# Performance work log

Hardware: AMD Instinct MI355X
Metric: run time of the kernel (lower is better)

Reference implementation:

```python
import jax, jax.numpy as jnp
import numpy as np

B, C_IN, C_OUT, H, W = 4, 256, 256, 64, 64
K, STRIDE, PAD, DIL = 3, 1, 1, 1
KK = K * K


def setup_inputs() -> dict:
    key = jax.random.key(0)
    k1, k2, k3, k4 = jax.random.split(key, 4)
    x = jax.random.normal(k1, (B, C_IN, H, W), jnp.float32)
    # offset/mask conv weight (no bias), scaled small so offsets are modest
    w_mod = jax.random.normal(k2, (3 * KK, C_IN, K, K), jnp.float32) * 0.01
    # deform conv weight (xavier-ish scale) + bias
    w_def = jax.random.normal(k3, (C_OUT, C_IN, K, K), jnp.float32) * (1.0 / np.sqrt(C_IN * KK))
    b_def = jax.random.normal(k4, (C_OUT,), jnp.float32) * 0.01
    return {"x": x, "w_mod": w_mod, "w_def": w_def, "b_def": b_def}


def _conv_nchw(x, w, stride, pad):
    return jax.lax.conv_general_dilated(
        x, w, (stride, stride), [(pad, pad), (pad, pad)],
        dimension_numbers=("NCHW", "OIHW", "NCHW"))


def _bilinear_sample(x, py, px):
    # x: [B,C,H,W]; py/px: [B,KK,Ho,Wo] absolute sample coords (zero-pad outside)
    Bn, Cc, Hh, Ww = x.shape
    y0 = jnp.floor(py)
    x0 = jnp.floor(px)
    fy = py - y0
    fx = px - x0
    y0i = y0.astype(jnp.int32)
    x0i = x0.astype(jnp.int32)
    xf = x.reshape(Bn, Cc, Hh * Ww)

    def corner(yi, xi, wgt):
        valid = (yi >= 0) & (yi < Hh) & (xi >= 0) & (xi < Ww)
        yc = jnp.clip(yi, 0, Hh - 1)
        xc = jnp.clip(xi, 0, Ww - 1)
        idx = yc * Ww + xc                      # [B,KK,Ho,Wo]
        g = jax.vmap(lambda f, i: f[:, i])(xf, idx)  # [B,C,KK,Ho,Wo]
        return g * (wgt * valid)[:, None]

    return (corner(y0i, x0i, (1 - fy) * (1 - fx))
            + corner(y0i, x0i + 1, (1 - fy) * fx)
            + corner(y0i + 1, x0i, fy * (1 - fx))
            + corner(y0i + 1, x0i + 1, fy * fx))


def reference(x, w_mod, w_def, b_def):
    # offset/mask head
    mod = _conv_nchw(x, w_mod, STRIDE, PAD)          # [B, 3*KK, Ho, Wo]
    o1, o2, mask = mod[:, :KK], mod[:, KK:2 * KK], mod[:, 2 * KK:]
    offset = jnp.concatenate([o1, o2], axis=1)        # [B, 2*KK, Ho, Wo]
    # torchvision DeformConv2d: offset channels are interleaved (y, x) pairs
    dy = offset[:, 0::2]
    dx = offset[:, 1::2]
    mask = jax.nn.sigmoid(mask)                       # [B, KK, Ho, Wo]

    Ho, Wo = mod.shape[2], mod.shape[3]
    ky, kx = jnp.meshgrid(jnp.arange(K), jnp.arange(K), indexing="ij")
    ky = ky.reshape(-1).astype(jnp.float32)
    kx = kx.reshape(-1).astype(jnp.float32)
    base_y = (jnp.arange(Ho, dtype=jnp.float32) * STRIDE - PAD)[None, :, None] + (ky * DIL)[:, None, None]  # [KK,Ho,1]
    base_x = (jnp.arange(Wo, dtype=jnp.float32) * STRIDE - PAD)[None, None, :] + (kx * DIL)[:, None, None]  # [KK,1,Wo]
    py = dy + base_y[None]                            # [B,KK,Ho,Wo]
    px = dx + base_x[None]

    sampled = _bilinear_sample(x, py, px) * mask[:, None]  # [B,C,KK,Ho,Wo]
    out = jnp.einsum("bckhw,ock->bohw", sampled, w_def.reshape(C_OUT, C_IN, KK))
    return out + b_def[None, :, None, None]
```

## Files before the change

kernel.cpp:

```cpp
#include <hip/hip_runtime.h>

typedef unsigned short u16;
typedef unsigned int u32;
typedef short bf16x8 __attribute__((ext_vector_type(8)));
typedef float f32x4 __attribute__((ext_vector_type(4)));

#define CIN 256
#define COUT 256

__device__ __forceinline__ u16 f2b(float f) {
  u32 u = __float_as_uint(f);
  u += 0x7fffu + ((u >> 16) & 1u);
  return (u16)(u >> 16);
}
__device__ __forceinline__ u32 packbf(float lo, float hi) {
  return (u32)f2b(lo) | ((u32)f2b(hi) << 16);
}
__device__ __forceinline__ u32 bil2(u32 u00, u32 u01, u32 u10, u32 u11, float4 wt) {
  float s0 = __uint_as_float(u00 << 16) * wt.x;
  s0 = fmaf(__uint_as_float(u01 << 16), wt.y, s0);
  s0 = fmaf(__uint_as_float(u10 << 16), wt.z, s0);
  s0 = fmaf(__uint_as_float(u11 << 16), wt.w, s0);
  float s1 = __uint_as_float(u00 & 0xffff0000u) * wt.x;
  s1 = fmaf(__uint_as_float(u01 & 0xffff0000u), wt.y, s1);
  s1 = fmaf(__uint_as_float(u10 & 0xffff0000u), wt.z, s1);
  s1 = fmaf(__uint_as_float(u11 & 0xffff0000u), wt.w, s1);
  return packbf(s0, s1);
}
__device__ __forceinline__ void bar() {
  asm volatile("s_waitcnt lgkmcnt(0)\n\ts_barrier" ::: "memory");
}

__global__ __launch_bounds__(256) void k_prep(
    const float* __restrict__ x, const float* __restrict__ w_mod,
    const float* __restrict__ w_def,
    u16* __restrict__ xT, u16* __restrict__ Wm2, u16* __restrict__ W2) {
  __shared__ __align__(16) char SB[9216];
  int t = threadIdx.x, g = blockIdx.x;
  if (g < 1024) {
    u16 (*T)[72] = (u16(*)[72])SB;
    int b = g >> 8, ct = (g >> 6) & 3, pt = g & 63;
    int c0 = ct << 6, pos0 = pt << 6;
    {
      int cl = t >> 2, pb = (t & 3) << 4;
      const float* p = x + (((b << 8) + c0 + cl) << 12) + pos0 + pb;
#pragma unroll
      for (int i = 0; i < 4; ++i) {
        float4 v = *(const float4*)(p + i * 4);
        int pp = pb + i * 4;
        T[pp][cl] = f2b(v.x); T[pp + 1][cl] = f2b(v.y);
        T[pp + 2][cl] = f2b(v.z); T[pp + 3][cl] = f2b(v.w);
      }
    }
    __syncthreads();
    {
      int pl = t >> 2, q = t & 3;
      u16* dst = xT + (((b << 12) + pos0 + pl) << 8) + c0 + (q << 4);
      *(uint4*)dst = *(const uint4*)&T[pl][q << 4];
      *(uint4*)(dst + 8) = *(const uint4*)&T[pl][(q << 4) + 8];
    }
  } else {
    float* L = (float*)SB;
    int gg = g - 1024;
    if (gg < 256) {
      const float* src = w_def + gg * 2304;
      for (int j = t; j < 2304; j += 256) L[j] = src[j];
      __syncthreads();
      u16* dst = W2 + gg * 2304;
      for (int j = t; j < 2304; j += 256) {
        int kk = j >> 8, c = j & 255;
        dst[j] = f2b(L[c * 9 + kk]);
      }
    } else {
      int cm = gg - 256;
      if (cm < 27) {
        const float* src = w_mod + cm * 2304;
        for (int j = t; j < 2304; j += 256) L[j] = src[j];
      }
      __syncthreads();
      u16* dst = Wm2 + cm * 2304;
      for (int j = t; j < 2304; j += 256) {
        int kk = j >> 8, c = j & 255;
        dst[j] = (cm < 27) ? f2b(L[c * 9 + kk]) : (u16)0;
      }
    }
  }
}

__global__ __launch_bounds__(512) void k_modconv(
    const u16* __restrict__ xT, const u16* __restrict__ Wm2,
    int2* __restrict__ cidx, float4* __restrict__ cwt) {
  __shared__ __align__(16) u16 As[2][2][64][72];
  __shared__ float mods2[2][32][66];
  int t = threadIdx.x;
  int l = t & 63;
  int w = t >> 6;
  int h = t >> 8;
  int wl = w & 3;
  int tg = t & 255;
  int px = tg >> 2, q = tg & 3;
  int g = blockIdx.x;
  int b = (g & 7) >> 1, y = ((g >> 3) << 1) + (g & 1);
  const u16* xTb = xT + (b << 20);
  f32x4 zero = {0.f, 0.f, 0.f, 0.f};
  f32x4 acc0 = zero, acc1 = zero;
  int ml = l & 15, kq = l >> 4;

  uint4 VA0, VA1, VB0, VB1;
  uint4 S0, S1, S2, S3, T0, T1, T2, T3;

#define MC_ISSUE_A(i, V0, V1)                                                \
  { int ch_ = h * 18 + (i); int kk_ = ch_ >> 2, c0_ = (ch_ & 3) << 6;        \
    int ky_ = kk_ / 3, kx_ = kk_ - 3 * ky_;                                  \
    int ys_ = y + ky_ - 1, xs_ = px + kx_ - 1;                               \
    V0 = make_uint4(0, 0, 0, 0); V1 = V0;                                    \
    if (ys_ >= 0 && ys_ < 64 && xs_ >= 0 && xs_ < 64) {                      \
      const u16* p_ = xTb + (((ys_ << 6) + xs_) << 8) + c0_ + (q << 4);      \
      V0 = *(const uint4*)p_; V1 = *(const uint4*)(p_ + 8);                  \
    } }

#define MC_ISSUE_B(i, R0, R1, R2, R3)                                        \
  { int ch_ = h * 18 + (i); int kk_ = ch_ >> 2, c0_ = (ch_ & 3) << 6;        \
    const u16* pw_ = Wm2 + (kk_ << 8) + c0_ + (kq << 3);                     \
    R0 = *(const uint4*)(pw_ + ml * 2304);                                   \
    R1 = *(const uint4*)(pw_ + (16 + ml) * 2304);                            \
    R2 = *(const uint4*)(pw_ + ml * 2304 + 32);                              \
    R3 = *(const uint4*)(pw_ + (16 + ml) * 2304 + 32); }

#define MC_WRITE(buf, V0, V1)                                                \
  { *(uint4*)&As[h][buf][px][q << 4] = V0;                                   \
    *(uint4*)&As[h][buf][px][(q << 4) + 8] = V1; }

#define MC_MFMA(buf, R0, R1, R2, R3)                                         \
  { bf16x8 a0_ = *(const bf16x8*)&As[h][buf][wl * 16 + ml][kq << 3];         \
    acc0 = __builtin_amdgcn_mfma_f32_16x16x32_bf16(a0_, *(const bf16x8*)&R0, acc0, 0,0,0); \
    acc1 = __builtin_amdgcn_mfma_f32_16x16x32_bf16(a0_, *(const bf16x8*)&R1, acc1, 0,0,0); \
    bf16x8 a1_ = *(const bf16x8*)&As[h][buf][wl * 16 + ml][32 + (kq << 3)];  \
    acc0 = __builtin_amdgcn_mfma_f32_16x16x32_bf16(a1_, *(const bf16x8*)&R2, acc0, 0,0,0); \
    acc1 = __builtin_amdgcn_mfma_f32_16x16x32_bf16(a1_, *(const bf16x8*)&R3, acc1, 0,0,0); }

  MC_ISSUE_A(0, VA0, VA1)
  MC_ISSUE_A(1, VB0, VB1)
  MC_ISSUE_B(0, S0, S1, S2, S3)
#pragma unroll 1
  for (int i2 = 0; i2 < 18; i2 += 2) {
    MC_WRITE(0, VA0, VA1)
    bar();
    if (i2 + 2 < 18) MC_ISSUE_A(i2 + 2, VA0, VA1)
    MC_ISSUE_B(i2 + 1, T0, T1, T2, T3)
    MC_MFMA(0, S0, S1, S2, S3)
    MC_WRITE(1, VB0, VB1)
    bar();
    if (i2 + 3 < 18) MC_ISSUE_A(i2 + 3, VB0, VB1)
    if (i2 + 2 < 18) MC_ISSUE_B(i2 + 2, S0, S1, S2, S3)
    MC_MFMA(1, T0, T1, T2, T3)
  }
#pragma unroll
  for (int r = 0; r < 4; ++r) {
    mods2[h][ml][wl * 16 + kq * 4 + r]      = acc0[r];
    mods2[h][16 + ml][wl * 16 + kq * 4 + r] = acc1[r];
  }
  __syncthreads();
  for (int i2 = t; i2 < 576; i2 += 512) {
    int kk = i2 >> 6, pxx_i = i2 & 63;
    float dy = mods2[0][2 * kk][pxx_i] + mods2[1][2 * kk][pxx_i];
    float dx = mods2[0][2 * kk + 1][pxx_i] + mods2[1][2 * kk + 1][pxx_i];
    float mv = mods2[0][18 + kk][pxx_i] + mods2[1][18 + kk][pxx_i];
    float msk = 1.f / (1.f + __expf(-mv));
    int ky = kk / 3, kx = kk - 3 * ky;
    float py  = dy + (float)(y + ky - 1);
    float pxx = dx + (float)(pxx_i + kx - 1);
    float y0f = floorf(py), x0f = floorf(pxx);
    float fy = py - y0f, fx = pxx - x0f;
    int y0 = (int)y0f, x0 = (int)x0f;
    float vy0 = (y0 >= 0 && y0 < 64) ? msk : 0.f;
    float vy1 = (y0 + 1 >= 0 && y0 + 1 < 64) ? msk : 0.f;
    float w00 = (1.f - fy) * (1.f - fx) * vy0;
    float w01 = (1.f - fy) * fx * vy0;
    float w10 = fy * (1.f - fx) * vy1;
    float w11 = fy * fx * vy1;
    int xb2 = min(max(x0, 0), 62);
    float wA0 = (xb2 == x0) ? w00 : ((xb2 == x0 + 1) ? w01 : 0.f);
    float wB0 = (xb2 + 1 == x0) ? w00 : ((xb2 + 1 == x0 + 1) ? w01 : 0.f);
    float wA1 = (xb2 == x0) ? w10 : ((xb2 == x0 + 1) ? w11 : 0.f);
    float wB1 = (xb2 + 1 == x0) ? w10 : ((xb2 + 1 == x0 + 1) ? w11 : 0.f);
    int ib0 = min(max(y0, 0), 63) * 64 + xb2;
    int ib1 = min(max(y0 + 1, 0), 63) * 64 + xb2;
    int ci = ((b * 9 + kk) << 12) + (y << 6) + pxx_i;
    cidx[ci] = make_int2(ib0, ib1);
    cwt[ci]  = make_float4(wA0, wB0, wA1, wB1);
  }
#undef MC_ISSUE_A
#undef MC_ISSUE_B
#undef MC_WRITE
#undef MC_MFMA
}

__global__ __launch_bounds__(512) void k_main(
    const u16* __restrict__ xT, const u16* __restrict__ W2,
    const float* __restrict__ b_def,
    const int2* __restrict__ cidx, const float4* __restrict__ cwt,
    float* __restrict__ out) {
  __shared__ __align__(16) u16 As[2][64][72];
  __shared__ __align__(16) int2 Cs_i[576];
  __shared__ __align__(16) float4 Cs_w[576];
  int t = threadIdx.x;
  int l = t & 63;
  int w = t >> 6;
  int g = blockIdx.x;
  int b = (g & 7) >> 1, y = ((g >> 3) << 1) + (g & 1);
  const u16* xTb = xT + (b << 20);
  int gm = t >> 3, go = t & 7;
  int ml = l & 15, kq = l >> 4;
  int nrow0 = w * 32 + ml, nrow1 = nrow0 + 16;

  f32x4 zero = {0.f, 0.f, 0.f, 0.f};
  f32x4 acc[4][2];
#pragma unroll
  for (int i = 0; i < 4; ++i) { acc[i][0] = zero; acc[i][1] = zero; }

  for (int i = t; i < 576; i += 512) {
    int kk = i >> 6, px = i & 63;
    int ci = ((b * 9 + kk) << 12) + (y << 6) + px;
    Cs_i[i] = cidx[ci];
    Cs_w[i] = cwt[ci];
  }
  bar();

  uint4 A00, A01, A02, A03; float4 wt0;
  uint4 A10, A11, A12, A13; float4 wt1;
  uint4 RA0, RA1, RA2, RA3;
  uint4 RB0, RB1, RB2, RB3;

#define ISSUE_A(chunk, a0, a1, a2, a3, wt)                                   \
  { int kk_ = (chunk) >> 2, c0_ = ((chunk) & 3) << 6;                        \
    int cI_ = (kk_ << 6) + gm;                                               \
    int2 ib_ = Cs_i[cI_];                                                    \
    wt = Cs_w[cI_];                                                          \
    const u16* p0_ = xTb + (ib_.x << 8) + c0_ + (go << 3);                   \
    const u16* p1_ = xTb + (ib_.y << 8) + c0_ + (go << 3);                   \
    a0 = *(const uint4*)p0_;  a1 = *(const uint4*)(p0_ + 256);               \
    a2 = *(const uint4*)p1_;  a3 = *(const uint4*)(p1_ + 256); }

#define ISSUE_B(chunk, R0, R1, R2, R3)                                       \
  { int kk_ = (chunk) >> 2, c0_ = ((chunk) & 3) << 6;                        \
    const u16* pw_ = W2 + (kk_ << 8) + c0_ + (kq << 3);                      \
    R0 = *(const uint4*)(pw_ + nrow0 * 2304);                                \
    R1 = *(const uint4*)(pw_ + nrow1 * 2304);                                \
    R2 = *(const uint4*)(pw_ + nrow0 * 2304 + 32);                           \
    R3 = *(const uint4*)(pw_ + nrow1 * 2304 + 32); }

#define UNPACK(CUR, a0, a1, a2, a3, wt)                                      \
  { u32 q0_ = bil2(a0.x, a1.x, a2.x, a3.x, wt);                              \
    u32 q1_ = bil2(a0.y, a1.y, a2.y, a3.y, wt);                              \
    u32 q2_ = bil2(a0.z, a1.z, a2.z, a3.z, wt);                              \
    u32 q3_ = bil2(a0.w, a1.w, a2.w, a3.w, wt);                              \
    *(uint4*)&As[CUR][gm][go << 3] = make_uint4(q0_, q1_, q2_, q3_); }

#define DOMFMA(CUR, R0, R1, R2, R3)                                          \
  { bf16x8 a0_ = *(const bf16x8*)&As[CUR][ml][kq << 3];                      \
    bf16x8 a1_ = *(const bf16x8*)&As[CUR][16 + ml][kq << 3];                 \
    bf16x8 a2_ = *(const bf16x8*)&As[CUR][32 + ml][kq << 3];                 \
    bf16x8 a3_ = *(const bf16x8*)&As[CUR][48 + ml][kq << 3];                 \
    bf16x8 b0_ = *(const bf16x8*)&R0;                                        \
    bf16x8 b1_ = *(const bf16x8*)&R1;                                        \
    acc[0][0] = __builtin_amdgcn_mfma_f32_16x16x32_bf16(a0_, b0_, acc[0][0], 0,0,0); \
    acc[1][0] = __builtin_amdgcn_mfma_f32_16x16x32_bf16(a1_, b0_, acc[1][0], 0,0,0); \
    acc[2][0] = __builtin_amdgcn_mfma_f32_16x16x32_bf16(a2_, b0_, acc[2][0], 0,0,0); \
    acc[3][0] = __builtin_amdgcn_mfma_f32_16x16x32_bf16(a3_, b0_, acc[3][0], 0,0,0); \
    acc[0][1] = __builtin_amdgcn_mfma_f32_16x16x32_bf16(a0_, b1_, acc[0][1], 0,0,0); \
    acc[1][1] = __builtin_amdgcn_mfma_f32_16x16x32_bf16(a1_, b1_, acc[1][1], 0,0,0); \
    acc[2][1] = __builtin_amdgcn_mfma_f32_16x16x32_bf16(a2_, b1_, acc[2][1], 0,0,0); \
    acc[3][1] = __builtin_amdgcn_mfma_f32_16x16x32_bf16(a3_, b1_, acc[3][1], 0,0,0); \
    a0_ = *(const bf16x8*)&As[CUR][ml][32 + (kq << 3)];                      \
    a1_ = *(const bf16x8*)&As[CUR][16 + ml][32 + (kq << 3)];                 \
    a2_ = *(const bf16x8*)&As[CUR][32 + ml][32 + (kq << 3)];                 \
    a3_ = *(const bf16x8*)&As[CUR][48 + ml][32 + (kq << 3)];                 \
    b0_ = *(const bf16x8*)&R2;                                               \
    b1_ = *(const bf16x8*)&R3;                                               \
    acc[0][0] = __builtin_amdgcn_mfma_f32_16x16x32_bf16(a0_, b0_, acc[0][0], 0,0,0); \
    acc[1][0] = __builtin_amdgcn_mfma_f32_16x16x32_bf16(a1_, b0_, acc[1][0], 0,0,0); \
    acc[2][0] = __builtin_amdgcn_mfma_f32_16x16x32_bf16(a2_, b0_, acc[2][0], 0,0,0); \
    acc[3][0] = __builtin_amdgcn_mfma_f32_16x16x32_bf16(a3_, b0_, acc[3][0], 0,0,0); \
    acc[0][1] = __builtin_amdgcn_mfma_f32_16x16x32_bf16(a0_, b1_, acc[0][1], 0,0,0); \
    acc[1][1] = __builtin_amdgcn_mfma_f32_16x16x32_bf16(a1_, b1_, acc[1][1], 0,0,0); \
    acc[2][1] = __builtin_amdgcn_mfma_f32_16x16x32_bf16(a2_, b1_, acc[2][1], 0,0,0); \
    acc[3][1] = __builtin_amdgcn_mfma_f32_16x16x32_bf16(a3_, b1_, acc[3][1], 0,0,0); }

  ISSUE_A(0, A00, A01, A02, A03, wt0)
  ISSUE_A(1, A10, A11, A12, A13, wt1)
  ISSUE_B(0, RA0, RA1, RA2, RA3)
#pragma unroll 1
  for (int c2 = 0; c2 < 36; c2 += 2) {
    UNPACK(0, A00, A01, A02, A03, wt0)
    bar();
    if (c2 + 2 < 36) ISSUE_A(c2 + 2, A00, A01, A02, A03, wt0)
    ISSUE_B(c2 + 1, RB0, RB1, RB2, RB3)
    DOMFMA(0, RA0, RA1, RA2, RA3)
    UNPACK(1, A10, A11, A12, A13, wt1)
    bar();
    if (c2 + 3 < 36) ISSUE_A(c2 + 3, A10, A11, A12, A13, wt1)
    if (c2 + 2 < 36) ISSUE_B(c2 + 2, RA0, RA1, RA2, RA3)
    DOMFMA(1, RB0, RB1, RB2, RB3)
  }

#pragma unroll
  for (int nt = 0; nt < 2; ++nt) {
    int n = w * 32 + nt * 16 + ml;
    float bias = b_def[n];
    float* op = out + (((b << 8) + n) << 12) + (y << 6);
#pragma unroll
    for (int mt = 0; mt < 4; ++mt) {
      float4 v;
      v.x = acc[mt][nt][0] + bias;
      v.y = acc[mt][nt][1] + bias;
      v.z = acc[mt][nt][2] + bias;
      v.w = acc[mt][nt][3] + bias;
      *(float4*)(op + mt * 16 + kq * 4) = v;
    }
  }
#undef ISSUE_A
#undef ISSUE_B
#undef UNPACK
#undef DOMFMA
}

extern "C" void kernel_launch(void* const* d_in, const int* in_sizes, int n_in,
                              void* d_out, int out_size, void* d_ws, size_t ws_size,
                              hipStream_t stream) {
  const float* x     = (const float*)d_in[0];
  const float* w_mod = (const float*)d_in[1];
  const float* w_def = (const float*)d_in[2];
  const float* b_def = (const float*)d_in[3];
  float* out = (float*)d_out;
  char* ws = (char*)d_ws;
  u16*    xT   = (u16*)(ws);
  u16*    W2   = (u16*)(ws + 8388608);
  u16*    Wm2  = (u16*)(ws + 8388608 + 1179648);
  int2*   cidx = (int2*)(ws + 8388608 + 1179648 + 147456);
  float4* cwt  = (float4*)(ws + 8388608 + 1179648 + 147456 + 1179648);

  hipLaunchKernelGGL(k_prep, dim3(1312), dim3(256), 0, stream, x, w_mod, w_def, xT, Wm2, W2);
  hipLaunchKernelGGL(k_modconv, dim3(256), dim3(512), 0, stream, xT, Wm2, cidx, cwt);
  hipLaunchKernelGGL(k_main, dim3(256), dim3(512), 0, stream, xT, W2, b_def, cidx, cwt, out);
}
```

Measured before the change: 158.2 us.

## Split output channels across two blocks to double k_main grid

k_main now launches 512 blocks instead of 256, and each block computes 128 output channels (16 per wave) instead of all 256. This gives more blocks per CU on a 256-CU part and halves the accumulator registers per wave. The cost is that the bilinear gather and unpack of the A tile is done twice, once per channel half, so global gather traffic and VALU work for sampling double. The workspace offsets are also moved into named constants, which does not change behaviour.

```diff
diff --git a/kernel.cpp b/kernel.cpp
--- a/kernel.cpp
+++ b/kernel.cpp
@@ -30,6 +30,12 @@
 __device__ __forceinline__ void bar() {
   asm volatile("s_waitcnt lgkmcnt(0)\n\ts_barrier" ::: "memory");
 }
+
+#define WS_XT    0u
+#define WS_W2    8388608u
+#define WS_WM2   9568256u
+#define WS_CIDX  9715712u
+#define WS_CWT   10895360u
 
 __global__ __launch_bounds__(256) void k_prep(
     const float* __restrict__ x, const float* __restrict__ w_mod,
@@ -208,16 +214,13 @@
   int l = t & 63;
   int w = t >> 6;
   int g = blockIdx.x;
-  int b = (g & 7) >> 1, y = ((g >> 3) << 1) + (g & 1);
+  int ns = g >> 8;
+  int r = g & 255;
+  int b = (r & 7) >> 1, y = ((r >> 3) << 1) + (r & 1);
   const u16* xTb = xT + (b << 20);
   int gm = t >> 3, go = t & 7;
   int ml = l & 15, kq = l >> 4;
-  int nrow0 = w * 32 + ml, nrow1 = nrow0 + 16;
-
-  f32x4 zero = {0.f, 0.f, 0.f, 0.f};
-  f32x4 acc[4][2];
-#pragma unroll
-  for (int i = 0; i < 4; ++i) { acc[i][0] = zero; acc[i][1] = zero; }
+  int nrow = ns * 128 + w * 16 + ml;
 
   for (int i = t; i < 576; i += 512) {
     int kk = i >> 6, px = i & 63;
@@ -225,12 +228,17 @@
     Cs_i[i] = cidx[ci];
     Cs_w[i] = cwt[ci];
   }
-  bar();
+  __syncthreads();
+
+  f32x4 zero = {0.f, 0.f, 0.f, 0.f};
+  f32x4 acc[4];
+#pragma unroll
+  for (int i = 0; i < 4; ++i) acc[i] = zero;
 
   uint4 A00, A01, A02, A03; float4 wt0;
   uint4 A10, A11, A12, A13; float4 wt1;
-  uint4 RA0, RA1, RA2, RA3;
-  uint4 RB0, RB1, RB2, RB3;
+  uint4 RA0, RA2;
+  uint4 RB0, RB2;
 
 #define ISSUE_A(chunk, a0, a1, a2, a3, wt)                                   \
   { int kk_ = (chunk) >> 2, c0_ = ((chunk) & 3) << 6;                        \
@@ -242,13 +250,11 @@
     a0 = *(const uint4*)p0_;  a1 = *(const uint4*)(p0_ + 256);               \
     a2 = *(const uint4*)p1_;  a3 = *(const uint4*)(p1_ + 256); }
 
-#define ISSUE_B(chunk, R0, R1, R2, R3)                                       \
+#define ISSUE_B(chunk, R0, R2)                                               \
   { int kk_ = (chunk) >> 2, c0_ = ((chunk) & 3) << 6;                        \
-    const u16* pw_ = W2 + (kk_ << 8) + c0_ + (kq << 3);                      \
-    R0 = *(const uint4*)(pw_ + nrow0 * 2304);                                \
-    R1 = *(const uint4*)(pw_ + nrow1 * 2304);                                \
-    R2 = *(const uint4*)(pw_ + nrow0 * 2304 + 32);                           \
-    R3 = *(const uint4*)(pw_ + nrow1 * 2304 + 32); }
+    const u16* pw_ = W2 + nrow * 2304 + (kk_ << 8) + c0_ + (kq << 3);        \
+    R0 = *(const uint4*)pw_;                                                 \
+    R2 = *(const uint4*)(pw_ + 32); }
 
 #define UNPACK(CUR, a0, a1, a2, a3, wt)                                      \
   { u32 q0_ = bil2(a0.x, a1.x, a2.x, a3.x, wt);                              \
@@ -257,65 +263,45 @@
     u32 q3_ = bil2(a0.w, a1.w, a2.w, a3.w, wt);                              \
     *(uint4*)&As[CUR][gm][go << 3] = make_uint4(q0_, q1_, q2_, q3_); }
 
-#define DOMFMA(CUR, R0, R1, R2, R3)                                          \
-  { bf16x8 a0_ = *(const bf16x8*)&As[CUR][ml][kq << 3];                      \
-    bf16x8 a1_ = *(const bf16x8*)&As[CUR][16 + ml][kq << 3];                 \
-    bf16x8 a2_ = *(const bf16x8*)&As[CUR][32 + ml][kq << 3];                 \
-    bf16x8 a3_ = *(const bf16x8*)&As[CUR][48 + ml][kq << 3];                 \
-    bf16x8 b0_ = *(const bf16x8*)&R0;                                        \
-    bf16x8 b1_ = *(const bf16x8*)&R1;                                        \
-    acc[0][0] = __builtin_amdgcn_mfma_f32_16x16x32_bf16(a0_, b0_, acc[0][0], 0,0,0); \
-    acc[1][0] = __builtin_amdgcn_mfma_f32_16x16x32_bf16(a1_, b0_, acc[1][0], 0,0,0); \
-    acc[2][0] = __builtin_amdgcn_mfma_f32_16x16x32_bf16(a2_, b0_, acc[2][0], 0,0,0); \
-    acc[3][0] = __builtin_amdgcn_mfma_f32_16x16x32_bf16(a3_, b0_, acc[3][0], 0,0,0); \
-    acc[0][1] = __builtin_amdgcn_mfma_f32_16x16x32_bf16(a0_, b1_, acc[0][1], 0,0,0); \
-    acc[1][1] = __builtin_amdgcn_mfma_f32_16x16x32_bf16(a1_, b1_, acc[1][1], 0,0,0); \
-    acc[2][1] = __builtin_amdgcn_mfma_f32_16x16x32_bf16(a2_, b1_, acc[2][1], 0,0,0); \
-    acc[3][1] = __builtin_amdgcn_mfma_f32_16x16x32_bf16(a3_, b1_, acc[3][1], 0,0,0); \
-    a0_ = *(const bf16x8*)&As[CUR][ml][32 + (kq << 3)];                      \
-    a1_ = *(const bf16x8*)&As[CUR][16 + ml][32 + (kq << 3)];                 \
-    a2_ = *(const bf16x8*)&As[CUR][32 + ml][32 + (kq << 3)];                 \
-    a3_ = *(const bf16x8*)&As[CUR][48 + ml][32 + (kq << 3)];                 \
-    b0_ = *(const bf16x8*)&R2;                                               \
-    b1_ = *(const bf16x8*)&R3;                                               \
-    acc[0][0] = __builtin_amdgcn_mfma_f32_16x16x32_bf16(a0_, b0_, acc[0][0], 0,0,0); \
-    acc[1][0] = __builtin_amdgcn_mfma_f32_16x16x32_bf16(a1_, b0_, acc[1][0], 0,0,0); \
-    acc[2][0] = __builtin_amdgcn_mfma_f32_16x16x32_bf16(a2_, b0_, acc[2][0], 0,0,0); \
-    acc[3][0] = __builtin_amdgcn_mfma_f32_16x16x32_bf16(a3_, b0_, acc[3][0], 0,0,0); \
-    acc[0][1] = __builtin_amdgcn_mfma_f32_16x16x32_bf16(a0_, b1_, acc[0][1], 0,0,0); \
-    acc[1][1] = __builtin_amdgcn_mfma_f32_16x16x32_bf16(a1_, b1_, acc[1][1], 0,0,0); \
-    acc[2][1] = __builtin_amdgcn_mfma_f32_16x16x32_bf16(a2_, b1_, acc[2][1], 0,0,0); \
-    acc[3][1] = __builtin_amdgcn_mfma_f32_16x16x32_bf16(a3_, b1_, acc[3][1], 0,0,0); }
+#define DOMFMA(CUR, R0, R2)                                                  \
+  { bf16x8 b0_ = *(const bf16x8*)&R0;                                        \
+    acc[0] = __builtin_amdgcn_mfma_f32_16x16x32_bf16(*(const bf16x8*)&As[CUR][ml][kq << 3],      b0_, acc[0], 0,0,0); \
+    acc[1] = __builtin_amdgcn_mfma_f32_16x16x32_bf16(*(const bf16x8*)&As[CUR][16 + ml][kq << 3], b0_, acc[1], 0,0,0); \
+    acc[2] = __builtin_amdgcn_mfma_f32_16x16x32_bf16(*(const bf16x8*)&As[CUR][32 + ml][kq << 3], b0_, acc[2], 0,0,0); \
+    acc[3] = __builtin_amdgcn_mfma_f32_16x16x32_bf16(*(const bf16x8*)&As[CUR][48 + ml][kq << 3], b0_, acc[3], 0,0,0); \
+    bf16x8 b1_ = *(const bf16x8*)&R2;                                        \
+    acc[0] = __builtin_amdgcn_mfma_f32_16x16x32_bf16(*(const bf16x8*)&As[CUR][ml][32 + (kq << 3)],      b1_, acc[0], 0,0,0); \
+    acc[1] = __builtin_amdgcn_mfma_f32_16x16x32_bf16(*(const bf16x8*)&As[CUR][16 + ml][32 + (kq << 3)], b1_, acc[1], 0,0,0); \
+    acc[2] = __builtin_amdgcn_mfma_f32_16x16x32_bf16(*(const bf16x8*)&As[CUR][32 + ml][32 + (kq << 3)], b1_, acc[2], 0,0,0); \
+    acc[3] = __builtin_amdgcn_mfma_f32_16x16x32_bf16(*(const bf16x8*)&As[CUR][48 + ml][32 + (kq << 3)], b1_, acc[3], 0,0,0); }
 
   ISSUE_A(0, A00, A01, A02, A03, wt0)
   ISSUE_A(1, A10, A11, A12, A13, wt1)
-  ISSUE_B(0, RA0, RA1, RA2, RA3)
+  ISSUE_B(0, RA0, RA2)
 #pragma unroll 1
   for (int c2 = 0; c2 < 36; c2 += 2) {
     UNPACK(0, A00, A01, A02, A03, wt0)
     bar();
     if (c2 + 2 < 36) ISSUE_A(c2 + 2, A00, A01, A02, A03, wt0)
-    ISSUE_B(c2 + 1, RB0, RB1, RB2, RB3)
-    DOMFMA(0, RA0, RA1, RA2, RA3)
+    ISSUE_B(c2 + 1, RB0, RB2)
+    DOMFMA(0, RA0, RA2)
     UNPACK(1, A10, A11, A12, A13, wt1)
     bar();
     if (c2 + 3 < 36) ISSUE_A(c2 + 3, A10, A11, A12, A13, wt1)
-    if (c2 + 2 < 36) ISSUE_B(c2 + 2, RA0, RA1, RA2, RA3)
-    DOMFMA(1, RB0, RB1, RB2, RB3)
-  }
-
-#pragma unroll
-  for (int nt = 0; nt < 2; ++nt) {
-    int n = w * 32 + nt * 16 + ml;
-    float bias = b_def[n];
-    float* op = out + (((b << 8) + n) << 12) + (y << 6);
+    if (c2 + 2 < 36) ISSUE_B(c2 + 2, RA0, RA2)
+    DOMFMA(1, RB0, RB2)
+  }
+
+  {
+    float bias = b_def[nrow];
+    float* op = out + (((b << 8) + nrow) << 12) + (y << 6);
 #pragma unroll
     for (int mt = 0; mt < 4; ++mt) {
       float4 v;
-      v.x = acc[mt][nt][0] + bias;
-      v.y = acc[mt][nt][1] + bias;
-      v.z = acc[mt][nt][2] + bias;
-      v.w = acc[mt][nt][3] + bias;
+      v.x = acc[mt][0] + bias;
+      v.y = acc[mt][1] + bias;
+      v.z = acc[mt][2] + bias;
+      v.w = acc[mt][3] + bias;
       *(float4*)(op + mt * 16 + kq * 4) = v;
     }
   }
@@ -334,13 +320,13 @@
   const float* b_def = (const float*)d_in[3];
   float* out = (float*)d_out;
   char* ws = (char*)d_ws;
-  u16*    xT   = (u16*)(ws);
-  u16*    W2   = (u16*)(ws + 8388608);
-  u16*    Wm2  = (u16*)(ws + 8388608 + 1179648);
-  int2*   cidx = (int2*)(ws + 8388608 + 1179648 + 147456);
-  float4* cwt  = (float4*)(ws + 8388608 + 1179648 + 147456 + 1179648);
+  u16*    xT   = (u16*)(ws + WS_XT);
+  u16*    W2   = (u16*)(ws + WS_W2);
+  u16*    Wm2  = (u16*)(ws + WS_WM2);
+  int2*   cidx = (int2*)(ws + WS_CIDX);
+  float4* cwt  = (float4*)(ws + WS_CWT);
 
   hipLaunchKernelGGL(k_prep, dim3(1312), dim3(256), 0, stream, x, w_mod, w_def, xT, Wm2, W2);
   hipLaunchKernelGGL(k_modconv, dim3(256), dim3(512), 0, stream, xT, Wm2, cidx, cwt);
-  hipLaunchKernelGGL(k_main, dim3(256), dim3(512), 0, stream, xT, W2, b_def, cidx, cwt, out);
-}
+  hipLaunchKernelGGL(k_main, dim3(512), dim3(512), 0, stream, xT, W2, b_def, cidx, cwt, out);
+}
```

Result: slower. 164.7 us (+4.1%).
